# Kernel optimization log

Measured on AMD Instinct MI355X. Metric: run time of the kernel, lower is better.

The kernel has to match this reference:

```python
import jax, jax.numpy as jnp
import numpy as np
import math

B, N, K, H = 2, 2048, 1024, 16
S = K // H  # head dim = 64


def apply_rope(t):
    # t: [b, h, N, s] -> rotary position embedding (rotate-half convention)
    s = t.shape[-1]
    pos = jnp.arange(t.shape[2], dtype=jnp.float32)
    inv_freq = 1.0 / (10000.0 ** (jnp.arange(0, s, 2, dtype=jnp.float32) / s))
    ang = pos[:, None] * inv_freq[None, :]               # [N, s/2]
    cos = jnp.concatenate([jnp.cos(ang), jnp.cos(ang)], axis=-1)  # [N, s]
    sin = jnp.concatenate([jnp.sin(ang), jnp.sin(ang)], axis=-1)
    t1, t2 = t[..., : s // 2], t[..., s // 2:]
    rot = jnp.concatenate([-t2, t1], axis=-1)
    return t * cos + rot * sin


def setup_inputs() -> dict:
    key = jax.random.key(0)
    ks = jax.random.split(key, 6)
    sc = 1.0 / math.sqrt(K)
    x = jax.random.normal(ks[0], (B, N, K), dtype=jnp.float32)
    Wq = jax.random.normal(ks[1], (K, K), dtype=jnp.float32) * sc
    Wk = jax.random.normal(ks[2], (K, K), dtype=jnp.float32) * sc
    Wv = jax.random.normal(ks[3], (K, K), dtype=jnp.float32) * sc
    Wu = jax.random.normal(ks[4], (K, K), dtype=jnp.float32) * sc
    bu = jax.random.normal(ks[5], (K,), dtype=jnp.float32) * 0.01
    mask = jnp.tril(jnp.ones((N, N), dtype=jnp.int32))  # causal
    return {"x": x, "Wq": Wq, "Wk": Wk, "Wv": Wv, "Wu": Wu, "bu": bu, "mask": mask}


def reference(x, Wq, Wk, Wv, Wu, bu, mask):
    b, n, k = x.shape
    h, s = H, S
    # torch Linear: y = x @ W.T
    def proj(W):
        return (x @ W.T).reshape(b, n, h, s).transpose(0, 2, 1, 3)  # [b,h,n,s]
    Q = apply_rope(proj(Wq))
    Kh = apply_rope(proj(Wk))
    V = proj(Wv)
    scores = jnp.einsum('bhqs,bhks->bhqk', Q, Kh) / math.sqrt(s)
    scores = jnp.where(mask[None, None, :, :] == 0, -jnp.inf, scores)
    attn = jax.nn.softmax(scores, axis=-1)
    out = jnp.einsum('bhqk,bhks->bhqs', attn, V)           # [b,h,n,s]
    out = out.transpose(0, 2, 1, 3).reshape(b, n, k)
    return out @ Wu.T + bu
```

## Files before the change

kernel.cpp:

```cpp
#include <hip/hip_runtime.h>
#include <hip/hip_bf16.h>

#define Bq 2
#define Nq 2048
#define Kq 1024
#define Hq 16
#define Sq 64
#define Mq (Bq * Nq)

typedef __attribute__((ext_vector_type(4))) float f32x4;
typedef __attribute__((ext_vector_type(8))) short bf16x8;

__device__ unsigned short g_xb[(size_t)Mq * Kq];
__device__ unsigned short g_Wqb[Kq * Kq];
__device__ unsigned short g_Wkb[Kq * Kq];
__device__ unsigned short g_Wvb[Kq * Kq];
__device__ unsigned short g_Wub[Kq * Kq];
__device__ unsigned short g_Qb[(size_t)Bq * Hq * Nq * Sq];
__device__ unsigned short g_Kb[(size_t)Bq * Hq * Nq * Sq];
__device__ unsigned short g_Vb[(size_t)Bq * Hq * Nq * Sq];
__device__ unsigned short g_Vt[(size_t)Bq * Hq * Sq * Nq];
__device__ unsigned short g_Ao[(size_t)Mq * Kq];

__device__ __forceinline__ unsigned short f2bf(float f) {
    union { float f; unsigned int i; } u; u.f = f;
    unsigned int r = u.i + 0x7FFF + ((u.i >> 16) & 1);
    return (unsigned short)(r >> 16);
}
__device__ __forceinline__ float bf2f(unsigned short u) {
    union { unsigned int i; float f; } v; v.i = ((unsigned int)u) << 16;
    return v.f;
}
__device__ __forceinline__ void async16(const unsigned short* g, unsigned short* l) {
    __builtin_amdgcn_global_load_lds(
        (const __attribute__((address_space(1))) void*)g,
        (__attribute__((address_space(3))) void*)l, 16, 0, 0);
}

__global__ __launch_bounds__(256) void convert_all_kernel(
    const float* __restrict__ x,  const float* __restrict__ wq,
    const float* __restrict__ wk, const float* __restrict__ wv,
    const float* __restrict__ wu)
{
    int i = blockIdx.x * 256 + threadIdx.x;
    const float* src; unsigned short* dst; int off;
    if (i < 1048576) { src = x; dst = g_xb; off = i; }
    else {
        int j = i - 1048576;
        int which = j >> 18;
        off = j & 262143;
        src = (which == 0) ? wq : (which == 1) ? wk : (which == 2) ? wv : wu;
        dst = (which == 0) ? g_Wqb : (which == 1) ? g_Wkb : (which == 2) ? g_Wvb : g_Wub;
    }
    float4 v = ((const float4*)src)[off];
    ushort4 o;
    o.x = f2bf(v.x); o.y = f2bf(v.y); o.z = f2bf(v.z); o.w = f2bf(v.w);
    ((ushort4*)dst)[off] = o;
}

__global__ __launch_bounds__(256) void qkv_gemm_kernel()
{
    __shared__ __align__(16) unsigned short As[2][128][64];
    __shared__ __align__(16) unsigned short Bs[2][128][64];

    const int n0 = blockIdx.x * 128;
    const int m0 = blockIdx.y * 128;
    const int which = n0 >> 10;
    const unsigned short* A  = g_xb;
    const unsigned short* Bm = (which == 0) ? g_Wqb : (which == 1) ? g_Wkb : g_Wvb;
    unsigned short* dst      = (which == 0) ? g_Qb : (which == 1) ? g_Kb : g_Vb;
    const int nb = n0 & 1023;

    const int tid = threadIdx.x;
    const int w = tid >> 6, l = tid & 63;
    const int lane16 = l & 15, quad = l >> 4;
    const int wm = (w >> 1) * 64, wn = (w & 1) * 64;

    const int sr = l >> 3;
    const int sc = ((l & 7) ^ sr) * 8;
    const int rsw = (lane16 & 7);

    f32x4 acc[4][4];
#pragma unroll
    for (int mi = 0; mi < 4; ++mi)
#pragma unroll
        for (int ni = 0; ni < 4; ++ni) acc[mi][ni] = (f32x4){0.f, 0.f, 0.f, 0.f};

#pragma unroll
    for (int c = 0; c < 4; ++c) {
        async16(A  + (size_t)(m0 + 32 * w + 8 * c + sr) * Kq + sc, &As[0][32 * w + 8 * c][0]);
        async16(Bm + (size_t)(nb + 32 * w + 8 * c + sr) * Kq + sc, &Bs[0][32 * w + 8 * c][0]);
    }
    __syncthreads();

    int cur = 0;
    for (int kt = 0; kt < Kq; kt += 64) {
        if (kt + 64 < Kq) {
            int nxt = cur ^ 1;
#pragma unroll
            for (int c = 0; c < 4; ++c) {
                async16(A  + (size_t)(m0 + 32 * w + 8 * c + sr) * Kq + kt + 64 + sc, &As[nxt][32 * w + 8 * c][0]);
                async16(Bm + (size_t)(nb + 32 * w + 8 * c + sr) * Kq + kt + 64 + sc, &Bs[nxt][32 * w + 8 * c][0]);
            }
        }
#pragma unroll
        for (int ks = 0; ks < 2; ++ks) {
            bf16x8 af[4], bfr[4];
#pragma unroll
            for (int mi = 0; mi < 4; ++mi)
                af[mi]  = *(const bf16x8*)&As[cur][wm + mi * 16 + lane16][((ks * 4 + quad) ^ rsw) * 8];
#pragma unroll
            for (int ni = 0; ni < 4; ++ni)
                bfr[ni] = *(const bf16x8*)&Bs[cur][wn + ni * 16 + lane16][((ks * 4 + quad) ^ rsw) * 8];
#pragma unroll
            for (int mi = 0; mi < 4; ++mi)
#pragma unroll
                for (int ni = 0; ni < 4; ++ni)
                    acc[mi][ni] = __builtin_amdgcn_mfma_f32_16x16x32_bf16(af[mi], bfr[ni], acc[mi][ni], 0, 0, 0);
        }
        __syncthreads();
        cur ^= 1;
    }

#pragma unroll
    for (int mi = 0; mi < 4; ++mi)
#pragma unroll
        for (int ni = 0; ni < 4; ++ni)
#pragma unroll
            for (int r = 0; r < 4; ++r) {
                int m = m0 + wm + mi * 16 + quad * 4 + r;
                int n = n0 + wn + ni * 16 + lane16;
                unsigned short v = f2bf(acc[mi][ni][r]);
                int b = m >> 11, nn = m & 2047;
                int o = n & 1023, h = o >> 6, s = o & 63;
                dst[(((size_t)b * Hq + h) * Nq + nn) * Sq + s] = v;
            }
}

__global__ __launch_bounds__(256) void rope_vtrans_kernel()
{
    __shared__ unsigned short T[64][72];

    if (blockIdx.y < 2) {
        unsigned short* buf = (blockIdx.y == 0) ? g_Qb : g_Kb;
        const int idx = blockIdx.x * 256 + threadIdx.x;
        const int i  = idx & 31;
        const int n  = (idx >> 5) & (Nq - 1);
        const int bh = idx >> 16;
        const size_t base = ((size_t)bh * Nq + n) * Sq + i;

        float t1 = bf2f(buf[base]);
        float t2 = bf2f(buf[base + 32]);
        float inv_freq = exp2f((float)i * -0.41524101f);
        float ang = (float)n * inv_freq;
        float sn = __sinf(ang), cs = __cosf(ang);
        buf[base]      = f2bf(t1 * cs - t2 * sn);
        buf[base + 32] = f2bf(t2 * cs + t1 * sn);
    } else {
        if (blockIdx.x >= 1024) return;
        const int n0 = (blockIdx.x & 31) * 64;
        const int bh = blockIdx.x >> 5;
        const unsigned short* src = g_Vb + (size_t)bh * Nq * Sq;
        unsigned short* dst       = g_Vt + (size_t)bh * Sq * Nq;
        const int tid = threadIdx.x;
        const int r = tid >> 3, c8 = (tid & 7) * 8;

        uint4 a0 = *(const uint4*)(src + (size_t)(n0 + r) * Sq + c8);
        uint4 a1 = *(const uint4*)(src + (size_t)(n0 + r + 32) * Sq + c8);
        *(uint4*)&T[r][c8] = a0;
        *(uint4*)&T[r + 32][c8] = a1;
        __syncthreads();

        union { ushort4 u4[2]; unsigned short u[8]; } p0, p1;
#pragma unroll
        for (int j = 0; j < 8; ++j) { p0.u[j] = T[c8 + j][r]; p1.u[j] = T[c8 + j][r + 32]; }
        *(uint4*)(dst + (size_t)r * Nq + n0 + c8)        = *(uint4*)&p0;
        *(uint4*)(dst + (size_t)(r + 32) * Nq + n0 + c8) = *(uint4*)&p1;
    }
}

__global__ __launch_bounds__(512) void attn_kernel()
{
    const int bh = blockIdx.x;
    const int j  = blockIdx.y;
    const int qt = (j < 8) ? (15 - j) : (j - 8);
    const int q0 = qt * 128;
    const unsigned short* Qp = g_Qb + (size_t)bh * Nq * Sq;
    const unsigned short* Kp = g_Kb + (size_t)bh * Nq * Sq;
    const unsigned short* Vp = g_Vt + (size_t)bh * Sq * Nq;

    __shared__ __align__(16) unsigned short Ks[2][64][64];
    __shared__ __align__(16) unsigned short Vs[2][64][64];
    __shared__ __align__(16) unsigned short Ps[128][64];
    unsigned short* psf = &Ps[0][0];

    const int tid = threadIdx.x;
    const int w = tid >> 6, l = tid & 63;
    const int lane16 = l & 15, quad = l >> 4;
    const int sr = l >> 3;
    const int sc = ((l & 7) ^ sr) * 8;
    const int rsw = (lane16 & 7);

    bf16x8 be;
    {
        short o = (lane16 == 0) ? (short)0x3F80 : (short)0;
#pragma unroll
        for (int i = 0; i < 8; ++i) be[i] = o;
    }

    const int qlo = q0 + 16 * w;
    bf16x8 aq0 = *(const bf16x8*)(Qp + (size_t)(qlo + lane16) * Sq + quad * 8);
    bf16x8 aq1 = *(const bf16x8*)(Qp + (size_t)(qlo + lane16) * Sq + quad * 8 + 32);

    f32x4 Oacc[4];
    f32x4 Oext = (f32x4){0.f, 0.f, 0.f, 0.f};
#pragma unroll
    for (int ds = 0; ds < 4; ++ds) Oacc[ds] = (f32x4){0.f, 0.f, 0.f, 0.f};

    const float C1 = 0.18033688f;
    const float C2 = 11.54156036f;

    async16(Kp + (size_t)(8 * w + sr) * Sq + sc, &Ks[0][8 * w][0]);
    async16(Vp + (size_t)(8 * w + sr) * Nq + sc, &Vs[0][8 * w][0]);
    __syncthreads();

    const int ntiles = 2 * qt + 2;
    int cur = 0;
    for (int kb = 0; kb < ntiles; ++kb) {
        if (kb + 1 < ntiles) {
            int kn = (kb + 1) * 64;
            int nb2 = cur ^ 1;
            async16(Kp + (size_t)(kn + 8 * w + sr) * Sq + sc, &Ks[nb2][8 * w][0]);
            async16(Vp + (size_t)(8 * w + sr) * Nq + kn + sc, &Vs[nb2][8 * w][0]);
        }

        if (kb * 64 <= qlo + 15) {
            f32x4 S[4];
#pragma unroll
            for (int kc = 0; kc < 4; ++kc) S[kc] = (f32x4){0.f, 0.f, 0.f, 0.f};
#pragma unroll
            for (int kc = 0; kc < 4; ++kc) {
                const unsigned short* krow = &Ks[cur][kc * 16 + lane16][0];
                bf16x8 bk0 = *(const bf16x8*)&krow[(quad ^ rsw) * 8];
                bf16x8 bk1 = *(const bf16x8*)&krow[((4 + quad) ^ rsw) * 8];
                S[kc] = __builtin_amdgcn_mfma_f32_16x16x32_bf16(aq0, bk0, S[kc], 0, 0, 0);
                S[kc] = __builtin_amdgcn_mfma_f32_16x16x32_bf16(aq1, bk1, S[kc], 0, 0, 0);
            }

            const int qbase = qlo + quad * 4;
            if (kb * 64 + 63 > qlo) {
#pragma unroll
                for (int kc = 0; kc < 4; ++kc) {
                    int kpos = kb * 64 + kc * 16 + lane16;
#pragma unroll
                    for (int r = 0; r < 4; ++r)
                        S[kc][r] = (kpos <= qbase + r) ? exp2f(fmaf(S[kc][r], C1, -C2)) : 0.0f;
                }
            } else {
#pragma unroll
                for (int kc = 0; kc < 4; ++kc)
#pragma unroll
                    for (int r = 0; r < 4; ++r)
                        S[kc][r] = exp2f(fmaf(S[kc][r], C1, -C2));
            }

#pragma unroll
            for (int kc = 0; kc < 4; ++kc)
#pragma unroll
                for (int r = 0; r < 4; ++r) {
                    int prow = 16 * w + quad * 4 + r;
                    psf[(prow * 64 + kc * 16 + lane16) ^ ((prow & 7) << 3)] =
                        (unsigned short)(__float_as_uint(S[kc][r]) >> 16);
                }

            const int prow2 = 16 * w + lane16;
#pragma unroll
            for (int kk = 0; kk < 2; ++kk) {
                bf16x8 pa = *(const bf16x8*)(psf +
                    ((prow2 * 64 + kk * 32 + quad * 8) ^ (rsw << 3)));
#pragma unroll
                for (int ds = 0; ds < 4; ++ds) {
                    bf16x8 vb = *(const bf16x8*)&Vs[cur][ds * 16 + lane16][((kk * 4 + quad) ^ rsw) * 8];
                    Oacc[ds] = __builtin_amdgcn_mfma_f32_16x16x32_bf16(pa, vb, Oacc[ds], 0, 0, 0);
                }
                Oext = __builtin_amdgcn_mfma_f32_16x16x32_bf16(pa, be, Oext, 0, 0, 0);
            }
        }

        __syncthreads();
        cur ^= 1;
    }

    const int b = bh >> 4, h = bh & 15;
    float inv[4];
#pragma unroll
    for (int r = 0; r < 4; ++r) {
        float lr = __shfl(Oext[r], quad * 16, 64);
        inv[r] = 1.0f / lr;
    }
#pragma unroll
    for (int ds = 0; ds < 4; ++ds)
#pragma unroll
        for (int r = 0; r < 4; ++r) {
            int nn = qlo + quad * 4 + r;
            g_Ao[((size_t)b * Nq + nn) * Kq + h * Sq + ds * 16 + lane16] =
                f2bf(Oacc[ds][r] * inv[r]);
        }
}

__global__ __launch_bounds__(256) void out_gemm_kernel(
    const float* __restrict__ bu, float* __restrict__ out)
{
    __shared__ __align__(16) unsigned short As[2][128][64];
    __shared__ __align__(16) unsigned short Bs[2][128][64];

    const int n0 = blockIdx.x * 128;
    const int m0 = blockIdx.y * 128;

    const int tid = threadIdx.x;
    const int w = tid >> 6, l = tid & 63;
    const int lane16 = l & 15, quad = l >> 4;
    const int wm = (w >> 1) * 64, wn = (w & 1) * 64;
    const int sr = l >> 3;
    const int sc = ((l & 7) ^ sr) * 8;
    const int rsw = (lane16 & 7);

    f32x4 acc[4][4];
#pragma unroll
    for (int mi = 0; mi < 4; ++mi)
#pragma unroll
        for (int ni = 0; ni < 4; ++ni) acc[mi][ni] = (f32x4){0.f, 0.f, 0.f, 0.f};

#pragma unroll
    for (int c = 0; c < 4; ++c) {
        async16(g_Ao  + (size_t)(m0 + 32 * w + 8 * c + sr) * Kq + sc, &As[0][32 * w + 8 * c][0]);
        async16(g_Wub + (size_t)(n0 + 32 * w + 8 * c + sr) * Kq + sc, &Bs[0][32 * w + 8 * c][0]);
    }
    __syncthreads();

    int cur = 0;
    for (int kt = 0; kt < Kq; kt += 64) {
        if (kt + 64 < Kq) {
            int nxt = cur ^ 1;
#pragma unroll
            for (int c = 0; c < 4; ++c) {
                async16(g_Ao  + (size_t)(m0 + 32 * w + 8 * c + sr) * Kq + kt + 64 + sc, &As[nxt][32 * w + 8 * c][0]);
                async16(g_Wub + (size_t)(n0 + 32 * w + 8 * c + sr) * Kq + kt + 64 + sc, &Bs[nxt][32 * w + 8 * c][0]);
            }
        }
#pragma unroll
        for (int ks = 0; ks < 2; ++ks) {
            bf16x8 af[4], bfr[4];
#pragma unroll
            for (int mi = 0; mi < 4; ++mi)
                af[mi]  = *(const bf16x8*)&As[cur][wm + mi * 16 + lane16][((ks * 4 + quad) ^ rsw) * 8];
#pragma unroll
            for (int ni = 0; ni < 4; ++ni)
                bfr[ni] = *(const bf16x8*)&Bs[cur][wn + ni * 16 + lane16][((ks * 4 + quad) ^ rsw) * 8];
#pragma unroll
            for (int mi = 0; mi < 4; ++mi)
#pragma unroll
                for (int ni = 0; ni < 4; ++ni)
                    acc[mi][ni] = __builtin_amdgcn_mfma_f32_16x16x32_bf16(af[mi], bfr[ni], acc[mi][ni], 0, 0, 0);
        }
        __syncthreads();
        cur ^= 1;
    }

#pragma unroll
    for (int mi = 0; mi < 4; ++mi)
#pragma unroll
        for (int ni = 0; ni < 4; ++ni)
#pragma unroll
            for (int r = 0; r < 4; ++r) {
                int m = m0 + wm + mi * 16 + quad * 4 + r;
                int n = n0 + wn + ni * 16 + lane16;
                out[(size_t)m * Kq + n] = acc[mi][ni][r] + bu[n];
            }
}

extern "C" void kernel_launch(void* const* d_in, const int* in_sizes, int n_in,
                              void* d_out, int out_size, void* d_ws, size_t ws_size,
                              hipStream_t stream)
{
    const float* x  = (const float*)d_in[0];
    const float* Wq = (const float*)d_in[1];
    const float* Wk = (const float*)d_in[2];
    const float* Wv = (const float*)d_in[3];
    const float* Wu = (const float*)d_in[4];
    const float* bu = (const float*)d_in[5];
    float* out = (float*)d_out;

    convert_all_kernel<<<8192, 256, 0, stream>>>(x, Wq, Wk, Wv, Wu);
    qkv_gemm_kernel<<<dim3(24, 32), 256, 0, stream>>>();
    rope_vtrans_kernel<<<dim3(8192, 3), 256, 0, stream>>>();
    attn_kernel<<<dim3(32, 16), 512, 0, stream>>>();
    out_gemm_kernel<<<dim3(8, 32), 256, 0, stream>>>(bu, out);
}
```

Before: 219.3 us.

## Triple-buffer K/V tiles in attention with explicit vmcnt waits

Moves the attention kernel's K/V shared-memory staging from double to triple buffering, prefetching two tiles ahead. Raw s_waitcnt vmcnt plus s_barrier replace __syncthreads, so only the oldest loads are waited on. This aims to hide global-to-LDS latency behind MFMA work. It costs extra LDS, about 16KB, which may lower occupancy, and it relies on correct vmcnt accounting of the async loads.

```diff
diff --git a/kernel.cpp b/kernel.cpp
--- a/kernel.cpp
+++ b/kernel.cpp
@@ -189,8 +189,8 @@
     const unsigned short* Kp = g_Kb + (size_t)bh * Nq * Sq;
     const unsigned short* Vp = g_Vt + (size_t)bh * Sq * Nq;
 
-    __shared__ __align__(16) unsigned short Ks[2][64][64];
-    __shared__ __align__(16) unsigned short Vs[2][64][64];
+    __shared__ __align__(16) unsigned short Ks[3][64][64];
+    __shared__ __align__(16) unsigned short Vs[3][64][64];
     __shared__ __align__(16) unsigned short Ps[128][64];
     unsigned short* psf = &Ps[0][0];
 
@@ -211,6 +211,7 @@
     const int qlo = q0 + 16 * w;
     bf16x8 aq0 = *(const bf16x8*)(Qp + (size_t)(qlo + lane16) * Sq + quad * 8);
     bf16x8 aq1 = *(const bf16x8*)(Qp + (size_t)(qlo + lane16) * Sq + quad * 8 + 32);
+    asm volatile("" : "+v"(aq0), "+v"(aq1));
 
     f32x4 Oacc[4];
     f32x4 Oext = (f32x4){0.f, 0.f, 0.f, 0.f};
@@ -220,19 +221,24 @@
     const float C1 = 0.18033688f;
     const float C2 = 11.54156036f;
 
-    async16(Kp + (size_t)(8 * w + sr) * Sq + sc, &Ks[0][8 * w][0]);
-    async16(Vp + (size_t)(8 * w + sr) * Nq + sc, &Vs[0][8 * w][0]);
-    __syncthreads();
-
     const int ntiles = 2 * qt + 2;
+
+#define STAGE(t, b)                                                           \
+    do {                                                                      \
+        int kn_ = (t) * 64;                                                   \
+        async16(Kp + (size_t)(kn_ + 8 * w + sr) * Sq + sc, &Ks[(b)][8 * w][0]);\
+        async16(Vp + (size_t)(8 * w + sr) * Nq + kn_ + sc, &Vs[(b)][8 * w][0]);\
+    } while (0)
+
+    STAGE(0, 0);
+    STAGE(1, 1);
+    asm volatile("s_waitcnt vmcnt(2)" ::: "memory");
+    __builtin_amdgcn_s_barrier();
+    __builtin_amdgcn_sched_barrier(0);
+
     int cur = 0;
     for (int kb = 0; kb < ntiles; ++kb) {
-        if (kb + 1 < ntiles) {
-            int kn = (kb + 1) * 64;
-            int nb2 = cur ^ 1;
-            async16(Kp + (size_t)(kn + 8 * w + sr) * Sq + sc, &Ks[nb2][8 * w][0]);
-            async16(Vp + (size_t)(8 * w + sr) * Nq + kn + sc, &Vs[nb2][8 * w][0]);
-        }
+        if (kb + 2 < ntiles) STAGE(kb + 2, (kb + 2) % 3);
 
         if (kb * 64 <= qlo + 15) {
             f32x4 S[4];
@@ -287,9 +293,17 @@
             }
         }
 
-        __syncthreads();
-        cur ^= 1;
-    }
+        __builtin_amdgcn_sched_barrier(0);
+        if (kb + 2 < ntiles) {
+            asm volatile("s_waitcnt vmcnt(2)" ::: "memory");
+        } else {
+            asm volatile("s_waitcnt vmcnt(0)" ::: "memory");
+        }
+        __builtin_amdgcn_s_barrier();
+        __builtin_amdgcn_sched_barrier(0);
+        cur = (cur == 2) ? 0 : cur + 1;
+    }
+#undef STAGE
 
     const int b = bh >> 4, h = bh & 15;
     float inv[4];
```

After: 221.6 us. Within noise of the previous version (+1.0%).
